# Optimization experiments

Measured on AMD Instinct MI355X. Metric: run time of the kernel, lower is better.

Reference implementation:

```python
import jax, jax.numpy as jnp
import numpy as np

B, S, D, H, T = 128, 256, 256, 1024, 128  # batch, src_len, input/output_dim, hidden, target_len


def setup_inputs() -> dict:
    key = jax.random.key(0)
    ks = jax.random.split(key, 16)
    sc = 0.05

    def p(k, shape):
        return (jax.random.normal(k, shape, jnp.float32) * sc)

    return {
        "x": jax.random.normal(ks[0], (B, S, D), jnp.float32),
        "x_target": jax.random.normal(ks[1], (B, T, D), jnp.float32),
        # encoder bidirectional LSTM (1 layer): gates order i,f,g,o (PyTorch)
        "enc_Wih_f": p(ks[2], (4 * H, D)),  "enc_Whh_f": p(ks[3], (4 * H, H)), "enc_b_f": p(ks[4], (4 * H,)),
        "enc_Wih_b": p(ks[5], (4 * H, D)),  "enc_Whh_b": p(ks[6], (4 * H, H)), "enc_b_b": p(ks[7], (4 * H,)),
        # decoder bidirectional LSTM (1 layer)
        "dec_Wih_f": p(ks[8], (4 * H, D)),  "dec_Whh_f": p(ks[9], (4 * H, H)), "dec_b_f": p(ks[10], (4 * H,)),
        "dec_Wih_b": p(ks[11], (4 * H, D)), "dec_Whh_b": p(ks[12], (4 * H, H)), "dec_b_b": p(ks[13], (4 * H,)),
        # decoder head: Linear(2H -> D)
        "mlp_W": p(ks[14], (D, 2 * H)), "mlp_b": p(ks[15], (D,)),
    }


def lstm_cell(x, h, c, Wih, Whh, b):
    # x: [B, Din], h/c: [B, H]; PyTorch gate order i, f, g, o
    g = x @ Wih.T + h @ Whh.T + b
    i, f, gg, o = jnp.split(g, 4, axis=-1)
    c = jax.nn.sigmoid(f) * c + jax.nn.sigmoid(i) * jnp.tanh(gg)
    h = jax.nn.sigmoid(o) * jnp.tanh(c)
    return h, c


def run_dir(xs, Wih, Whh, b, reverse):
    # xs: [S, B, Din]; returns final (h, c) for one direction (zero init, like torch LSTM without h0)
    h0 = jnp.zeros((xs.shape[1], Whh.shape[1]), xs.dtype)
    c0 = jnp.zeros_like(h0)

    def step(carry, xt):
        h, c = lstm_cell(xt, *carry, Wih, Whh, b)
        return (h, c), None

    (h, c), _ = jax.lax.scan(step, (h0, c0), xs, reverse=reverse)
    return h, c


def reference(x, x_target, enc_Wih_f, enc_Whh_f, enc_b_f, enc_Wih_b, enc_Whh_b, enc_b_b,
              dec_Wih_f, dec_Whh_f, dec_b_f, dec_Wih_b, dec_Whh_b, dec_b_b, mlp_W, mlp_b):
    xs = jnp.transpose(x, (1, 0, 2))  # [S, B, D], time-major
    hf, cf = run_dir(xs, enc_Wih_f, enc_Whh_f, enc_b_f, reverse=False)
    hb, cb = run_dir(xs, enc_Wih_b, enc_Whh_b, enc_b_b, reverse=True)

    dec_in = x[:, -1, :]  # [B, D]

    def step(carry, _):
        hf, cf, hb, cb, inp = carry
        # bidirectional LSTM on a length-1 sequence: both directions see the same step
        hf2, cf2 = lstm_cell(inp, hf, cf, dec_Wih_f, dec_Whh_f, dec_b_f)
        hb2, cb2 = lstm_cell(inp, hb, cb, dec_Wih_b, dec_Whh_b, dec_b_b)
        out = jnp.concatenate([hf2, hb2], axis=-1) @ mlp_W.T + mlp_b  # [B, D]
        # teacher_forcing_ratio = 0.0 -> always feed model output back
        return (hf2, cf2, hb2, cb2, out), out

    _, outs = jax.lax.scan(step, (hf, cf, hb, cb, dec_in), None, length=T)
    return jnp.transpose(outs, (1, 0, 2))  # [B, T, D]
```

## Files before the change

kernel.cpp:

```cpp
#include <hip/hip_runtime.h>
#include <stdint.h>


typedef __attribute__((ext_vector_type(8))) short bfx8;
typedef __attribute__((ext_vector_type(4))) float f32x4;
typedef __attribute__((ext_vector_type(4))) unsigned short u16x4;
typedef unsigned short ushort_t;
typedef unsigned long long u64;

#define NWG 256
#define MFMA(a,b,c) __builtin_amdgcn_mfma_f32_16x16x32_bf16((a),(b),(c),0,0,0)
#define WAITVM(N) { asm volatile("s_waitcnt vmcnt(" #N ")" ::: "memory"); __builtin_amdgcn_sched_barrier(0); }
#define WAITLG(N) { asm volatile("s_waitcnt lgkmcnt(" #N ")" ::: "memory"); __builtin_amdgcn_sched_barrier(0); }
#define SBAR()    { __builtin_amdgcn_s_barrier(); __builtin_amdgcn_sched_barrier(0); }

__device__ __forceinline__ unsigned short f2bf(float f){
  unsigned u = __float_as_uint(f);
  u += 0x7FFFu + ((u >> 16) & 1u);
  return (unsigned short)(u >> 16);
}
__device__ __forceinline__ float bf2f(unsigned short h){
  return __uint_as_float(((unsigned)h) << 16);
}
__device__ __forceinline__ float sigm(float x){ return 1.f/(1.f + __expf(-x)); }
__device__ __forceinline__ float tanh_(float x){ return 1.f - 2.f/(__expf(2.f*x) + 1.f); }

__device__ __forceinline__ void stage16(const void* g, void* l){
  __builtin_amdgcn_global_load_lds((const __attribute__((address_space(1))) void*)g,
                                   (__attribute__((address_space(3))) void*)l,
                                   16, 0, 0);
}
__device__ __forceinline__ void stage16c(const void* g, void* l){
  __builtin_amdgcn_global_load_lds((const __attribute__((address_space(1))) void*)g,
                                   (__attribute__((address_space(3))) void*)l,
                                   16, 0, 0x11);
}

__device__ __forceinline__ bfx8 ld16c(const ushort_t* p){
  const u64* q = (const u64*)p;
  u64 a = __hip_atomic_load(q,     __ATOMIC_RELAXED, __HIP_MEMORY_SCOPE_AGENT);
  u64 b = __hip_atomic_load(q + 1, __ATOMIC_RELAXED, __HIP_MEMORY_SCOPE_AGENT);
  union { u64 u[2]; bfx8 v; } x; x.u[0] = a; x.u[1] = b; return x.v;
}
__device__ __forceinline__ void sth2(ushort_t* p, unsigned short v){
  __hip_atomic_store(p, v, __ATOMIC_RELAXED, __HIP_MEMORY_SCOPE_AGENT);
}

__device__ __forceinline__ void cvt2(const f32x4& a, const f32x4& b, bfx8& hi, bfx8& lo){
#pragma unroll
  for (int j = 0; j < 4; ++j){
    unsigned short h0 = f2bf(a[j]);
    unsigned short h1 = f2bf(b[j]);
    hi[j]   = (short)h0; lo[j]   = (short)f2bf(a[j] - bf2f(h0));
    hi[4+j] = (short)h1; lo[4+j] = (short)f2bf(b[j] - bf2f(h1));
  }
}

__device__ __forceinline__ void bar(unsigned* flags, int nflags, int me, unsigned gen){
  __syncthreads();
  if (threadIdx.x == 0)
    __hip_atomic_store(&flags[me], gen, __ATOMIC_RELAXED, __HIP_MEMORY_SCOPE_AGENT);
  if (threadIdx.x < 64){
    const int l = threadIdx.x;
    for (;;){
      unsigned mn = 0xFFFFFFFFu;
      for (int o = l; o < nflags; o += 64){
        unsigned v = __hip_atomic_load(&flags[o], __ATOMIC_RELAXED, __HIP_MEMORY_SCOPE_AGENT);
        mn = mn < v ? mn : v;
      }
      if (__all((int)(mn >= gen))) break;
      __builtin_amdgcn_s_sleep(1);
    }
  }
  __syncthreads();
}

struct Frags { bfx8 awh0, awh1, awl0, awl1, bh0, bh1, bl0, bl1; };

template<int ENC>
__device__ __forceinline__ void cell_step(
    const float*    __restrict__ Wih,
    const ushort_t* __restrict__ WhH,
    const ushort_t* __restrict__ WhL,
    const float*    __restrict__ bias,
    const float*    __restrict__ xsl,
    const ushort_t* __restrict__ iph,
    const ushort_t* __restrict__ ipl,
    const ushort_t* __restrict__ hh,
    const ushort_t* __restrict__ hl,
    ushort_t* __restrict__ outh, ushort_t* __restrict__ outl,
    float (&creg)[2][2],
    int r0, int n0, int b0, ushort_t* LDS)
{
  const int tid  = threadIdx.x;
  const int lane = tid & 63;
  const int wv   = tid >> 6;
  const int wm   = wv >> 1, wn = wv & 1;
  const int lr   = tid >> 3;
  const int lc   = tid & 7;
  const int cb   = lane >> 4;
  const int fr   = lane & 15;
  const int sc8  = lc ^ (lr & 7);
  const int sx   = fr & 7;
  const int rwa0 = wm*32 + fr, rwa1 = rwa0 + 16;
  const int rwb0 = wn*32 + fr, rwb1 = rwb0 + 16;

  const int ra = r0 + lr, rb = ra + 32;
  const float* wih0 = Wih + (size_t)((ra & 3)*1024 + (ra >> 2))*256 + sc8*8;
  const float* wih1 = Wih + (size_t)((rb & 3)*1024 + (rb >> 2))*256 + sc8*8;
  const float *xs0 = nullptr, *xs1 = nullptr;
  const ushort_t *ih0 = nullptr, *ih1 = nullptr, *il0 = nullptr, *il1 = nullptr;
  if (ENC){
    xs0 = xsl + (size_t)(b0 + lr)*65536 + sc8*8;
    xs1 = xs0 + (size_t)32*65536;
  } else {
    ih0 = iph + (size_t)(b0 + lr)*256 + sc8*8;  ih1 = ih0 + 32*256;
    il0 = ipl + (size_t)(b0 + lr)*256 + sc8*8;  il1 = il0 + 32*256;
  }

  const ushort_t* sb; size_t sstr; int srow0;
  if      (wv == 0){ sb = WhH; sstr = 1024; srow0 = r0; }
  else if (wv == 1){ sb = WhL; sstr = 1024; srow0 = r0; }
  else if (wv == 2){ sb = hh;  sstr = 2048; srow0 = b0; }
  else             { sb = hl;  sstr = 2048; srow0 = b0; }
  const int srw = lane >> 3;
  const int sg  = (lane & 7) ^ srw;
  const ushort_t* pj[8];
#pragma unroll
  for (int j = 0; j < 8; ++j)
    pj[j] = sb + (size_t)(srow0 + j*8 + srw)*sstr + sg*8;
  ushort_t* ldsb[3];
#pragma unroll
  for (int bp = 0; bp < 3; ++bp)
    ldsb[bp] = LDS + 16384 + bp*16384 + wv*4096;

  auto ISSUE = [&](int c, int bp){
    const int ko = (c - 4)*64;
    if (wv < 2){
#pragma unroll
      for (int j = 0; j < 8; ++j)
        stage16(pj[j] + ko, ldsb[bp] + j*512);
    } else {
#pragma unroll
      for (int j = 0; j < 8; ++j)
        stage16c(pj[j] + ko, ldsb[bp] + j*512);
    }
  };

  f32x4 acc[2][2] = {};
  auto rdf = [&](const ushort_t* buf, int ks, Frags& f){
    const int ga = (((ks << 2) + cb) ^ sx) << 3;
    f.awh0 = *(const bfx8*)(buf +         rwa0*64 + ga);
    f.awh1 = *(const bfx8*)(buf +         rwa1*64 + ga);
    f.awl0 = *(const bfx8*)(buf + 4096  + rwa0*64 + ga);
    f.awl1 = *(const bfx8*)(buf + 4096  + rwa1*64 + ga);
    f.bh0  = *(const bfx8*)(buf + 8192  + rwb0*64 + ga);
    f.bh1  = *(const bfx8*)(buf + 8192  + rwb1*64 + ga);
    f.bl0  = *(const bfx8*)(buf + 12288 + rwb0*64 + ga);
    f.bl1  = *(const bfx8*)(buf + 12288 + rwb1*64 + ga);
  };
  auto mm12 = [&](const Frags& f){
    acc[0][0] = MFMA(f.awh0, f.bh0, acc[0][0]);
    acc[0][0] = MFMA(f.awh0, f.bl0, acc[0][0]);
    acc[0][0] = MFMA(f.awl0, f.bh0, acc[0][0]);
    acc[0][1] = MFMA(f.awh0, f.bh1, acc[0][1]);
    acc[0][1] = MFMA(f.awh0, f.bl1, acc[0][1]);
    acc[0][1] = MFMA(f.awl0, f.bh1, acc[0][1]);
    acc[1][0] = MFMA(f.awh1, f.bh0, acc[1][0]);
    acc[1][0] = MFMA(f.awh1, f.bl0, acc[1][0]);
    acc[1][0] = MFMA(f.awl1, f.bh0, acc[1][0]);
    acc[1][1] = MFMA(f.awh1, f.bh1, acc[1][1]);
    acc[1][1] = MFMA(f.awh1, f.bl1, acc[1][1]);
    acc[1][1] = MFMA(f.awl1, f.bh1, acc[1][1]);
  };

  f32x4 rw0a, rw0b, rw1a, rw1b, rxa0, rxb0, rxa1, rxb1;
  bfx8 cwh0, cwh1, cwl0, cwl1, cah0, cah1, cal0, cal1;
  auto LOADRAW = [&](int kc){
    rw0a = *(const f32x4*)(wih0 + kc);  rw0b = *(const f32x4*)(wih0 + kc + 4);
    rw1a = *(const f32x4*)(wih1 + kc);  rw1b = *(const f32x4*)(wih1 + kc + 4);
    if (ENC){
      rxa0 = *(const f32x4*)(xs0 + kc); rxb0 = *(const f32x4*)(xs0 + kc + 4);
      rxa1 = *(const f32x4*)(xs1 + kc); rxb1 = *(const f32x4*)(xs1 + kc + 4);
    } else {
      cah0 = ld16c(ih0 + kc);  cah1 = ld16c(ih1 + kc);
      cal0 = ld16c(il0 + kc);  cal1 = ld16c(il1 + kc);
    }
  };
  auto CVT = [&](){
    cvt2(rw0a, rw0b, cwh0, cwl0);
    cvt2(rw1a, rw1b, cwh1, cwl1);
    if (ENC){ cvt2(rxa0, rxb0, cah0, cal0); cvt2(rxa1, rxb1, cah1, cal1); }
  };

  LOADRAW(0);
  ISSUE(4, 0); ISSUE(5, 1); ISSUE(6, 2);
  CVT();

  for (int c = 0; c < 4; ++c){
    *(bfx8*)(LDS +         lr    *64 + lc*8) = cwh0;
    *(bfx8*)(LDS +        (lr+32)*64 + lc*8) = cwh1;
    *(bfx8*)(LDS + 4096 +  lr    *64 + lc*8) = cwl0;
    *(bfx8*)(LDS + 4096 + (lr+32)*64 + lc*8) = cwl1;
    *(bfx8*)(LDS + 8192 +  lr    *64 + lc*8) = cah0;
    *(bfx8*)(LDS + 8192 + (lr+32)*64 + lc*8) = cah1;
    *(bfx8*)(LDS + 12288 + lr    *64 + lc*8) = cal0;
    *(bfx8*)(LDS + 12288 +(lr+32)*64 + lc*8) = cal1;
    WAITLG(0); SBAR();
    if (c < 3) LOADRAW((c + 1)*64);
    Frags f0, f1;
    rdf(LDS, 0, f0);
    rdf(LDS, 1, f1);
    WAITLG(8);
    mm12(f0);
    WAITLG(0); SBAR();
    if (c < 3) CVT();
    mm12(f1);
  }

  int bi = 0;
  for (int i = 4; i <= 19; ++i){
    if (i < 18)      { WAITVM(16); }
    else if (i == 18){ WAITVM(8); }
    else             { WAITVM(0); }
    SBAR();
    const ushort_t* buf = LDS + 16384 + bi*16384;
    Frags f0, f1;
    rdf(buf, 0, f0);
    rdf(buf, 1, f1);
    WAITLG(8);
    mm12(f0);
    WAITLG(0); SBAR();
    if (i <= 16) ISSUE(i + 3, bi);
    mm12(f1);
    bi = (bi == 2) ? 0 : bi + 1;
  }

#pragma unroll
  for (int m = 0; m < 2; ++m){
    const int n = n0 + wm*8 + m*4 + cb;
    const float bi_ = bias[n];
    const float bf_ = bias[1024 + n];
    const float bg_ = bias[2048 + n];
    const float bo_ = bias[3072 + n];
#pragma unroll
    for (int nb = 0; nb < 2; ++nb){
      const int b = b0 + wn*32 + nb*16 + fr;
      float gi = acc[m][nb][0] + bi_;
      float gf = acc[m][nb][1] + bf_;
      float gg = acc[m][nb][2] + bg_;
      float go = acc[m][nb][3] + bo_;
      float c_new = sigm(gf)*creg[m][nb] + sigm(gi)*tanh_(gg);
      float h_new = sigm(go)*tanh_(c_new);
      creg[m][nb] = c_new;
      unsigned short hi = f2bf(h_new);
      sth2(&outh[(size_t)b*2048 + n], hi);
      sth2(&outl[(size_t)b*2048 + n], f2bf(h_new - bf2f(hi)));
    }
  }
}

__device__ __forceinline__ void mlp_gemm(
    const ushort_t* __restrict__ hch, const ushort_t* __restrict__ hcl,
    const ushort_t* __restrict__ mWh, const ushort_t* __restrict__ mWl,
    float* __restrict__ Part, int wg, ushort_t* LDS)
{
  const int tid = threadIdx.x, lane = tid & 63, wv = tid >> 6;
  const int cb = lane >> 4, fr = lane & 15, sx = fr & 7;
  const int wgl = wg & 127, kh = wg >> 7;
  const int d0 = (wgl >> 3)*16, b0 = (wgl & 7)*16;
  const int kb = kh*1024 + wv*256;
  const int srw = lane >> 3, sg = (lane & 7) ^ srw;

  const ushort_t* ps[4] = { mWh, mWl, hch, hcl };
  const int pr0[4] = { d0, d0, b0, b0 };
  const ushort_t* pj[4][2];
#pragma unroll
  for (int p = 0; p < 4; ++p)
#pragma unroll
    for (int j = 0; j < 2; ++j)
      pj[p][j] = ps[p] + (size_t)(pr0[p] + j*8 + srw)*2048 + kb + sg*8;
  ushort_t* lb[3];
#pragma unroll
  for (int bp = 0; bp < 3; ++bp)
    lb[bp] = LDS + 16384 + (wv*3 + bp)*4096;

  auto ISSUE = [&](int c, int bp){
    const int ko = c*64;
#pragma unroll
    for (int p = 0; p < 4; ++p)
#pragma unroll
      for (int j = 0; j < 2; ++j){
        if (p < 2) stage16 (pj[p][j] + ko, lb[bp] + p*1024 + j*512);
        else       stage16c(pj[p][j] + ko, lb[bp] + p*1024 + j*512);
      }
  };
  ISSUE(0, 0); ISSUE(1, 1); ISSUE(2, 2);

  f32x4 acc = {};
  int bp = 0;
  for (int c = 0; c < 4; ++c){
    if (c < 2)      { WAITVM(16); }
    else if (c == 2){ WAITVM(8); }
    else            { WAITVM(0); }
    const ushort_t* B = lb[bp];
    const int ga0 = ((cb) ^ sx) << 3;
    const int ga1 = ((4 + cb) ^ sx) << 3;
    bfx8 wh0 = *(const bfx8*)(B +        fr*64 + ga0);
    bfx8 wl0 = *(const bfx8*)(B + 1024 + fr*64 + ga0);
    bfx8 ah0 = *(const bfx8*)(B + 2048 + fr*64 + ga0);
    bfx8 al0 = *(const bfx8*)(B + 3072 + fr*64 + ga0);
    bfx8 wh1 = *(const bfx8*)(B +        fr*64 + ga1);
    bfx8 wl1 = *(const bfx8*)(B + 1024 + fr*64 + ga1);
    bfx8 ah1 = *(const bfx8*)(B + 2048 + fr*64 + ga1);
    bfx8 al1 = *(const bfx8*)(B + 3072 + fr*64 + ga1);
    WAITLG(0);
    if (c == 0) ISSUE(3, 0);
    acc = MFMA(wh0, ah0, acc); acc = MFMA(wh0, al0, acc); acc = MFMA(wl0, ah0, acc);
    acc = MFMA(wh1, ah1, acc); acc = MFMA(wh1, al1, acc); acc = MFMA(wl1, ah1, acc);
    bp = (bp == 2) ? 0 : bp + 1;
  }
  u64* P8 = (u64*)Part;
  const size_t idx = (((size_t)wgl*2 + kh)*4 + wv)*64 + lane;
  u64 a = ((u64)__float_as_uint(acc[1]) << 32) | __float_as_uint(acc[0]);
  u64 b = ((u64)__float_as_uint(acc[3]) << 32) | __float_as_uint(acc[2]);
  __hip_atomic_store(&P8[2*idx],     a, __ATOMIC_RELAXED, __HIP_MEMORY_SCOPE_AGENT);
  __hip_atomic_store(&P8[2*idx + 1], b, __ATOMIC_RELAXED, __HIP_MEMORY_SCOPE_AGENT);
}

__device__ __forceinline__ void mlp_combine(
    const float* __restrict__ Part, const float* __restrict__ mb,
    float* __restrict__ dout,
    ushort_t* __restrict__ inph, ushort_t* __restrict__ inpl, int wg, int t)
{
  if (threadIdx.x >= 64) return;
  const int lane = threadIdx.x;
  const int d0 = (wg >> 3)*16, b0 = (wg & 7)*16;
  const int cb = lane >> 4, fr = lane & 15;
  const u64* P8 = (const u64*)Part;
  f32x4 s = {};
#pragma unroll
  for (int kh = 0; kh < 2; ++kh)
#pragma unroll
    for (int wv = 0; wv < 4; ++wv){
      const size_t idx = (((size_t)wg*2 + kh)*4 + wv)*64 + lane;
      u64 a = __hip_atomic_load(&P8[2*idx],     __ATOMIC_RELAXED, __HIP_MEMORY_SCOPE_AGENT);
      u64 b = __hip_atomic_load(&P8[2*idx + 1], __ATOMIC_RELAXED, __HIP_MEMORY_SCOPE_AGENT);
      s[0] += __uint_as_float((unsigned)a);
      s[1] += __uint_as_float((unsigned)(a >> 32));
      s[2] += __uint_as_float((unsigned)b);
      s[3] += __uint_as_float((unsigned)(b >> 32));
    }
  const int dr = d0 + cb*4, b = b0 + fr;
  s += *(const f32x4*)&mb[dr];
  *(f32x4*)&dout[((size_t)b*128 + t)*256 + dr] = s;
  u16x4 hv, lv;
#pragma unroll
  for (int j = 0; j < 4; ++j){
    hv[j] = f2bf(s[j]);
    lv[j] = f2bf(s[j] - bf2f(hv[j]));
  }
  union { u16x4 v; u64 u; } ch, cl; ch.v = hv; cl.v = lv;
  __hip_atomic_store((u64*)&inph[(size_t)b*256 + dr], ch.u, __ATOMIC_RELAXED, __HIP_MEMORY_SCOPE_AGENT);
  __hip_atomic_store((u64*)&inpl[(size_t)b*256 + dr], cl.u, __ATOMIC_RELAXED, __HIP_MEMORY_SCOPE_AGENT);
}

__device__ __forceinline__ void wg_decode(int wg, int& dir, int& r0, int& n0,
                                          int& b0, int& me){
  const int half = (wg >> 3) & 1;
  const int rgd  = (wg & 7) | ((wg >> 4) << 3);
  dir = rgd >> 6;
  const int rg = rgd & 63;
  r0 = rg * 64; n0 = rg * 16; b0 = half * 64;
  me = (rg << 1) | half;
}

__global__ void __launch_bounds__(256) rnn_enc_kernel(
    const float* __restrict__ Wih_f, const float* __restrict__ b_f,
    const float* __restrict__ Wih_b, const float* __restrict__ b_b,
    const ushort_t* __restrict__ WhhH, const ushort_t* __restrict__ WhhL,
    const float* __restrict__ x,
    ushort_t* __restrict__ Hh, ushort_t* __restrict__ Hl,
    float* __restrict__ C, unsigned* flagsE)
{
  extern __shared__ ushort_t LDS[];
  int dir, r0, n0, b0, me;
  wg_decode(blockIdx.x, dir, r0, n0, b0, me);
  const float* Wih = dir ? Wih_b : Wih_f;
  const float* bia = dir ? b_b : b_f;
  const ushort_t* WhH = WhhH + (size_t)dir*4096*1024;
  const ushort_t* WhL = WhhL + (size_t)dir*4096*1024;
  unsigned* fl = flagsE + dir*128;
  float creg[2][2] = {{0.f, 0.f}, {0.f, 0.f}};
  unsigned gen = 0;
  for (int t = 0; t < 256; ++t){
    const int tt = dir ? (255 - t) : t;
    const int rp = t & 1;
    cell_step<1>(Wih, WhH, WhL, bia,
                 x + (size_t)tt*256, nullptr, nullptr,
                 Hh + (size_t)rp     *262144 + dir*1024,
                 Hl + (size_t)rp     *262144 + dir*1024,
                 Hh + (size_t)(rp^1) *262144 + dir*1024,
                 Hl + (size_t)(rp^1) *262144 + dir*1024,
                 creg, r0, n0, b0, LDS);
    ++gen;
    bar(fl, 128, me, gen);
  }
  {
    const int lane = threadIdx.x & 63, wv = threadIdx.x >> 6;
    const int wm = wv >> 1, wn = wv & 1, cb = lane >> 4, fr = lane & 15;
    float* Cst = C + (size_t)dir*1024*128;
#pragma unroll
    for (int m = 0; m < 2; ++m)
#pragma unroll
      for (int nb = 0; nb < 2; ++nb){
        const int n = n0 + wm*8 + m*4 + cb;
        const int b = b0 + wn*32 + nb*16 + fr;
        Cst[n*128 + b] = creg[m][nb];
      }
  }
}

__global__ void __launch_bounds__(256) rnn_dec_kernel(
    const float* __restrict__ Wih_f, const float* __restrict__ b_f,
    const float* __restrict__ Wih_b, const float* __restrict__ b_b,
    const ushort_t* __restrict__ WhhH, const ushort_t* __restrict__ WhhL,
    const ushort_t* __restrict__ mWh, const ushort_t* __restrict__ mWl,
    const float* __restrict__ mb,
    ushort_t* __restrict__ Hh, ushort_t* __restrict__ Hl,
    float* __restrict__ C,
    ushort_t* __restrict__ inph, ushort_t* __restrict__ inpl,
    float* __restrict__ Part,
    float* __restrict__ dout, unsigned* flagsD)
{
  extern __shared__ ushort_t LDS[];
  const int wg = blockIdx.x;
  int dir, r0, n0, b0, me;
  wg_decode(wg, dir, r0, n0, b0, me);
  const float* Wih = dir ? Wih_b : Wih_f;
  const float* bia = dir ? b_b : b_f;
  const ushort_t* WhH = WhhH + (size_t)dir*4096*1024;
  const ushort_t* WhL = WhhL + (size_t)dir*4096*1024;
  float creg[2][2];
  {
    const int lane = threadIdx.x & 63, wv = threadIdx.x >> 6;
    const int wm = wv >> 1, wn = wv & 1, cb = lane >> 4, fr = lane & 15;
    const float* Cst = C + (size_t)dir*1024*128;
#pragma unroll
    for (int m = 0; m < 2; ++m)
#pragma unroll
      for (int nb = 0; nb < 2; ++nb){
        const int n = n0 + wm*8 + m*4 + cb;
        const int b = b0 + wn*32 + nb*16 + fr;
        creg[m][nb] = Cst[n*128 + b];
      }
  }
  for (int t = 0; t < 128; ++t){
    const int rp = t & 1;
    cell_step<0>(Wih, WhH, WhL, bia,
                 nullptr, inph, inpl,
                 Hh + (size_t)rp     *262144 + dir*1024,
                 Hl + (size_t)rp     *262144 + dir*1024,
                 Hh + (size_t)(rp^1) *262144 + dir*1024,
                 Hl + (size_t)(rp^1) *262144 + dir*1024,
                 creg, r0, n0, b0, LDS);
    bar(flagsD, 256, wg, (unsigned)(3*t + 1));
    mlp_gemm(Hh + (size_t)(rp^1)*262144, Hl + (size_t)(rp^1)*262144,
             mWh, mWl, Part, wg, LDS);
    bar(flagsD, 256, wg, (unsigned)(3*t + 2));
    if (wg < 128) mlp_combine(Part, mb, dout, inph, inpl, wg, t);
    bar(flagsD, 256, wg, (unsigned)(3*t + 3));
  }
}

__global__ void k_wplanes(ushort_t* Hp, ushort_t* Lp,
                          const float* Whh_f, const float* Whh_b)
{
  const size_t N = 2ull*4096*1024;
  for (size_t i = (size_t)blockIdx.x*blockDim.x + threadIdx.x; i < N;
       i += (size_t)gridDim.x*blockDim.x){
    int dir = (int)(i >> 22);
    int r   = (int)((i >> 10) & 4095);
    int k   = (int)(i & 1023);
    int n = r >> 2, q = r & 3;
    const float* W = dir ? Whh_b : Whh_f;
    float v = W[(size_t)(q*1024 + n)*1024 + k];
    unsigned short h = f2bf(v);
    Hp[i] = h;
    Lp[i] = f2bf(v - bf2f(h));
  }
}

__global__ void k_init(ushort_t* Hh, ushort_t* Hl,
                       ushort_t* inph, ushort_t* inpl,
                       ushort_t* mWh, ushort_t* mWl,
                       const float* x, const float* mW, unsigned* cnt)
{
  const size_t N = 524288;
  for (size_t i = (size_t)blockIdx.x*blockDim.x + threadIdx.x; i < N;
       i += (size_t)gridDim.x*blockDim.x){
    Hh[i] = 0; Hl[i] = 0;
    float wv = mW[i];
    unsigned short wh = f2bf(wv);
    mWh[i] = wh;
    mWl[i] = f2bf(wv - bf2f(wh));
    if (i < 32768){
      int b = (int)(i >> 8), d = (int)(i & 255);
      float v = x[((size_t)b*256 + 255)*256 + d];
      unsigned short hi = f2bf(v);
      inph[i] = hi;
      inpl[i] = f2bf(v - bf2f(hi));
    }
    if (i < 1024) cnt[i] = 0;
  }
}

extern "C" void kernel_launch(void* const* d_in, const int* in_sizes, int n_in,
                              void* d_out, int out_size, void* d_ws, size_t ws_size,
                              hipStream_t stream)
{
  (void)in_sizes; (void)n_in; (void)out_size; (void)ws_size;
  const float* x      = (const float*)d_in[0];
  const float* eWih_f = (const float*)d_in[2];
  const float* eWhh_f = (const float*)d_in[3];
  const float* eb_f   = (const float*)d_in[4];
  const float* eWih_b = (const float*)d_in[5];
  const float* eWhh_b = (const float*)d_in[6];
  const float* eb_b   = (const float*)d_in[7];
  const float* dWih_f = (const float*)d_in[8];
  const float* dWhh_f = (const float*)d_in[9];
  const float* db_f   = (const float*)d_in[10];
  const float* dWih_b = (const float*)d_in[11];
  const float* dWhh_b = (const float*)d_in[12];
  const float* db_b   = (const float*)d_in[13];
  const float* mW     = (const float*)d_in[14];
  const float* mb     = (const float*)d_in[15];

  char* p = (char*)d_ws;
  size_t off = 0;
  unsigned* cnt   = (unsigned*)(p + off);  off += 4096;
  ushort_t* WhhEh = (ushort_t*)(p + off);  off += 16777216;
  ushort_t* WhhEl = (ushort_t*)(p + off);  off += 16777216;
  ushort_t* WhhDh = (ushort_t*)(p + off);  off += 16777216;
  ushort_t* WhhDl = (ushort_t*)(p + off);  off += 16777216;
  ushort_t* mWh   = (ushort_t*)(p + off);  off += 1048576;
  ushort_t* mWl   = (ushort_t*)(p + off);  off += 1048576;
  ushort_t* Hh    = (ushort_t*)(p + off);  off += 1048576;
  ushort_t* Hl    = (ushort_t*)(p + off);  off += 1048576;
  float*    C     = (float*)(p + off);     off += 1048576;
  ushort_t* inph  = (ushort_t*)(p + off);  off += 65536;
  ushort_t* inpl  = (ushort_t*)(p + off);  off += 65536;
  float*    Part  = (float*)(p + off);     off += 1048576;

  unsigned* flagsD = cnt;
  unsigned* flagsE = cnt + 256;

  hipFuncSetAttribute(reinterpret_cast<const void*>(rnn_enc_kernel),
                      hipFuncAttributeMaxDynamicSharedMemorySize, 131072);
  hipFuncSetAttribute(reinterpret_cast<const void*>(rnn_dec_kernel),
                      hipFuncAttributeMaxDynamicSharedMemorySize, 131072);

  k_init   <<<512, 256, 0, stream>>>(Hh, Hl, inph, inpl, mWh, mWl, x, mW, cnt);
  k_wplanes<<<2048, 256, 0, stream>>>(WhhEh, WhhEl, eWhh_f, eWhh_b);
  k_wplanes<<<2048, 256, 0, stream>>>(WhhDh, WhhDl, dWhh_f, dWhh_b);

  rnn_enc_kernel<<<NWG, 256, 131072, stream>>>(eWih_f, eb_f, eWih_b, eb_b,
                                               WhhEh, WhhEl, x, Hh, Hl, C, flagsE);
  rnn_dec_kernel<<<NWG, 256, 131072, stream>>>(dWih_f, db_f, dWih_b, db_b,
                                               WhhDh, WhhDl, mWh, mWl, mb,
                                               Hh, Hl, C, inph, inpl, Part,
                                               (float*)d_out, flagsD);
}
```

Before: 10.12 ms.

## Replicate hidden state into per-XCC scratch copies to avoid coherent cross-die loads

New measurement: 24.89 ms. 2.46x slower.

```diff
diff --git a/kernel.cpp b/kernel.cpp
--- a/kernel.cpp
+++ b/kernel.cpp
@@ -34,6 +34,11 @@
   __builtin_amdgcn_global_load_lds((const __attribute__((address_space(1))) void*)g,
                                    (__attribute__((address_space(3))) void*)l,
                                    16, 0, 0x11);
+}
+__device__ __forceinline__ void stage16s(const void* g, void* l){
+  __builtin_amdgcn_global_load_lds((const __attribute__((address_space(1))) void*)g,
+                                   (__attribute__((address_space(3))) void*)l,
+                                   16, 0, 0x1);
 }
 
 __device__ __forceinline__ bfx8 ld16c(const ushort_t* p){
@@ -75,9 +80,71 @@
   __syncthreads();
 }
 
+__device__ __forceinline__ void xreg(unsigned* regc, int grp, int& xcc, int& rank){
+  __shared__ unsigned s0, s1;
+  if (threadIdx.x == 0){
+    unsigned x;
+    asm volatile("s_getreg_b32 %0, hwreg(HW_REG_XCC_ID)" : "=s"(x));
+    x &= 7u;
+    s0 = x;
+    s1 = atomicAdd(&regc[(grp*8 + (int)x)*16], 1u);
+  }
+  __syncthreads();
+  xcc = (int)s0; rank = (int)s1;
+}
+__device__ __forceinline__ int xnmem(unsigned* regc, int grp, int xcc){
+  __shared__ unsigned s;
+  if (threadIdx.x == 0)
+    s = __hip_atomic_load(&regc[(grp*8 + xcc)*16], __ATOMIC_RELAXED, __HIP_MEMORY_SCOPE_AGENT);
+  __syncthreads();
+  return (int)s;
+}
+__device__ __forceinline__ void xbar(unsigned* arr, unsigned* flag, int nmem, unsigned gen){
+  __syncthreads();
+  if (threadIdx.x == 0){
+    unsigned a = atomicAdd(arr, 1u);
+    if (a == gen*(unsigned)nmem - 1u)
+      __hip_atomic_store(flag, gen, __ATOMIC_RELAXED, __HIP_MEMORY_SCOPE_AGENT);
+    while (__hip_atomic_load(flag, __ATOMIC_RELAXED, __HIP_MEMORY_SCOPE_AGENT) < gen)
+      __builtin_amdgcn_s_sleep(1);
+  }
+  __syncthreads();
+}
+
+__device__ __forceinline__ void xcopy_half(
+    const ushort_t* Hs, const ushort_t* Ls, ushort_t* Hd, ushort_t* Ld,
+    int dir, int rank, int nmem){
+  for (int u = rank*256 + (int)threadIdx.x; u < 16384; u += nmem*256){
+    const size_t o = (size_t)(u >> 7)*2048 + (size_t)dir*1024 + (size_t)(u & 127)*8;
+    const u64* s1 = (const u64*)(Hs + o);
+    const u64* s2 = (const u64*)(Ls + o);
+    u64 a = __hip_atomic_load(s1,     __ATOMIC_RELAXED, __HIP_MEMORY_SCOPE_AGENT);
+    u64 b = __hip_atomic_load(s1 + 1, __ATOMIC_RELAXED, __HIP_MEMORY_SCOPE_AGENT);
+    u64 c = __hip_atomic_load(s2,     __ATOMIC_RELAXED, __HIP_MEMORY_SCOPE_AGENT);
+    u64 d = __hip_atomic_load(s2 + 1, __ATOMIC_RELAXED, __HIP_MEMORY_SCOPE_AGENT);
+    ((u64*)(Hd + o))[0] = a; ((u64*)(Hd + o))[1] = b;
+    ((u64*)(Ld + o))[0] = c; ((u64*)(Ld + o))[1] = d;
+  }
+}
+__device__ __forceinline__ void xcopy_full(
+    const ushort_t* Hs, const ushort_t* Ls, ushort_t* Hd, ushort_t* Ld,
+    int rank, int nmem){
+  for (int u = rank*256 + (int)threadIdx.x; u < 32768; u += nmem*256){
+    const size_t o = (size_t)u*8;
+    const u64* s1 = (const u64*)(Hs + o);
+    const u64* s2 = (const u64*)(Ls + o);
+    u64 a = __hip_atomic_load(s1,     __ATOMIC_RELAXED, __HIP_MEMORY_SCOPE_AGENT);
+    u64 b = __hip_atomic_load(s1 + 1, __ATOMIC_RELAXED, __HIP_MEMORY_SCOPE_AGENT);
+    u64 c = __hip_atomic_load(s2,     __ATOMIC_RELAXED, __HIP_MEMORY_SCOPE_AGENT);
+    u64 d = __hip_atomic_load(s2 + 1, __ATOMIC_RELAXED, __HIP_MEMORY_SCOPE_AGENT);
+    ((u64*)(Hd + o))[0] = a; ((u64*)(Hd + o))[1] = b;
+    ((u64*)(Ld + o))[0] = c; ((u64*)(Ld + o))[1] = d;
+  }
+}
+
 struct Frags { bfx8 awh0, awh1, awl0, awl1, bh0, bh1, bl0, bl1; };
 
-template<int ENC>
+template<int ENC, int COH>
 __device__ __forceinline__ void cell_step(
     const float*    __restrict__ Wih,
     const ushort_t* __restrict__ WhH,
@@ -140,10 +207,14 @@
 #pragma unroll
       for (int j = 0; j < 8; ++j)
         stage16(pj[j] + ko, ldsb[bp] + j*512);
-    } else {
+    } else if (COH){
 #pragma unroll
       for (int j = 0; j < 8; ++j)
         stage16c(pj[j] + ko, ldsb[bp] + j*512);
+    } else {
+#pragma unroll
+      for (int j = 0; j < 8; ++j)
+        stage16s(pj[j] + ko, ldsb[bp] + j*512);
     }
   };
 
@@ -292,7 +363,7 @@
 #pragma unroll
       for (int j = 0; j < 2; ++j){
         if (p < 2) stage16 (pj[p][j] + ko, lb[bp] + p*1024 + j*512);
-        else       stage16c(pj[p][j] + ko, lb[bp] + p*1024 + j*512);
+        else       stage16s(pj[p][j] + ko, lb[bp] + p*1024 + j*512);
       }
   };
   ISSUE(0, 0); ISSUE(1, 1); ISSUE(2, 2);
@@ -381,7 +452,9 @@
     const ushort_t* __restrict__ WhhH, const ushort_t* __restrict__ WhhL,
     const float* __restrict__ x,
     ushort_t* __restrict__ Hh, ushort_t* __restrict__ Hl,
-    float* __restrict__ C, unsigned* flagsE)
+    ushort_t* __restrict__ scrH, ushort_t* __restrict__ scrL,
+    float* __restrict__ C, unsigned* flagsE,
+    unsigned* eReg, unsigned* eArr, unsigned* eFlg)
 {
   extern __shared__ ushort_t LDS[];
   int dir, r0, n0, b0, me;
@@ -391,20 +464,32 @@
   const ushort_t* WhH = WhhH + (size_t)dir*4096*1024;
   const ushort_t* WhL = WhhL + (size_t)dir*4096*1024;
   unsigned* fl = flagsE + dir*128;
+
+  int xcc, rank;
+  xreg(eReg, dir, xcc, rank);
+  bar(fl, 128, me, 1);
+  const int nmem = xnmem(eReg, dir, xcc);
+  const ushort_t* sH = scrH + (size_t)xcc*262144;
+  const ushort_t* sL = scrL + (size_t)xcc*262144;
+  unsigned* xa = eArr + (dir*8 + xcc)*16;
+  unsigned* xf = eFlg + (dir*8 + xcc)*16;
+
   float creg[2][2] = {{0.f, 0.f}, {0.f, 0.f}};
-  unsigned gen = 0;
   for (int t = 0; t < 256; ++t){
     const int tt = dir ? (255 - t) : t;
     const int rp = t & 1;
-    cell_step<1>(Wih, WhH, WhL, bia,
-                 x + (size_t)tt*256, nullptr, nullptr,
-                 Hh + (size_t)rp     *262144 + dir*1024,
-                 Hl + (size_t)rp     *262144 + dir*1024,
-                 Hh + (size_t)(rp^1) *262144 + dir*1024,
-                 Hl + (size_t)(rp^1) *262144 + dir*1024,
-                 creg, r0, n0, b0, LDS);
-    ++gen;
-    bar(fl, 128, me, gen);
+    cell_step<1,0>(Wih, WhH, WhL, bia,
+                   x + (size_t)tt*256, nullptr, nullptr,
+                   sH + dir*1024, sL + dir*1024,
+                   Hh + (size_t)(rp^1)*262144 + dir*1024,
+                   Hl + (size_t)(rp^1)*262144 + dir*1024,
+                   creg, r0, n0, b0, LDS);
+    bar(fl, 128, me, (unsigned)(t + 2));
+    if (t < 255){
+      xcopy_half(Hh + (size_t)(rp^1)*262144, Hl + (size_t)(rp^1)*262144,
+                 (ushort_t*)sH, (ushort_t*)sL, dir, rank, nmem);
+      xbar(xa, xf, nmem, (unsigned)(t + 1));
+    }
   }
   {
     const int lane = threadIdx.x & 63, wv = threadIdx.x >> 6;
@@ -428,10 +513,12 @@
     const ushort_t* __restrict__ mWh, const ushort_t* __restrict__ mWl,
     const float* __restrict__ mb,
     ushort_t* __restrict__ Hh, ushort_t* __restrict__ Hl,
+    ushort_t* __restrict__ scrH, ushort_t* __restrict__ scrL,
     float* __restrict__ C,
     ushort_t* __restrict__ inph, ushort_t* __restrict__ inpl,
     float* __restrict__ Part,
-    float* __restrict__ dout, unsigned* flagsD)
+    float* __restrict__ dout, unsigned* flagsD,
+    unsigned* dReg, unsigned* dArr, unsigned* dFlg)
 {
   extern __shared__ ushort_t LDS[];
   const int wg = blockIdx.x;
@@ -441,6 +528,16 @@
   const float* bia = dir ? b_b : b_f;
   const ushort_t* WhH = WhhH + (size_t)dir*4096*1024;
   const ushort_t* WhL = WhhL + (size_t)dir*4096*1024;
+
+  int xcc, rank;
+  xreg(dReg, 0, xcc, rank);
+  bar(flagsD, 256, wg, 1);
+  const int nmem = xnmem(dReg, 0, xcc);
+  const ushort_t* sH = scrH + (size_t)xcc*262144;
+  const ushort_t* sL = scrL + (size_t)xcc*262144;
+  unsigned* xa = dArr + xcc*16;
+  unsigned* xf = dFlg + xcc*16;
+
   float creg[2][2];
   {
     const int lane = threadIdx.x & 63, wv = threadIdx.x >> 6;
@@ -457,19 +554,27 @@
   }
   for (int t = 0; t < 128; ++t){
     const int rp = t & 1;
-    cell_step<0>(Wih, WhH, WhL, bia,
-                 nullptr, inph, inpl,
-                 Hh + (size_t)rp     *262144 + dir*1024,
-                 Hl + (size_t)rp     *262144 + dir*1024,
-                 Hh + (size_t)(rp^1) *262144 + dir*1024,
-                 Hl + (size_t)(rp^1) *262144 + dir*1024,
-                 creg, r0, n0, b0, LDS);
-    bar(flagsD, 256, wg, (unsigned)(3*t + 1));
-    mlp_gemm(Hh + (size_t)(rp^1)*262144, Hl + (size_t)(rp^1)*262144,
-             mWh, mWl, Part, wg, LDS);
+    if (t == 0)
+      cell_step<0,1>(Wih, WhH, WhL, bia, nullptr, inph, inpl,
+                     Hh + (size_t)rp*262144 + dir*1024,
+                     Hl + (size_t)rp*262144 + dir*1024,
+                     Hh + (size_t)(rp^1)*262144 + dir*1024,
+                     Hl + (size_t)(rp^1)*262144 + dir*1024,
+                     creg, r0, n0, b0, LDS);
+    else
+      cell_step<0,0>(Wih, WhH, WhL, bia, nullptr, inph, inpl,
+                     sH + dir*1024, sL + dir*1024,
+                     Hh + (size_t)(rp^1)*262144 + dir*1024,
+                     Hl + (size_t)(rp^1)*262144 + dir*1024,
+                     creg, r0, n0, b0, LDS);
     bar(flagsD, 256, wg, (unsigned)(3*t + 2));
+    xcopy_full(Hh + (size_t)(rp^1)*262144, Hl + (size_t)(rp^1)*262144,
+               (ushort_t*)sH, (ushort_t*)sL, rank, nmem);
+    xbar(xa, xf, nmem, (unsigned)(t + 1));
+    mlp_gemm(sH, sL, mWh, mWl, Part, wg, LDS);
+    bar(flagsD, 256, wg, (unsigned)(3*t + 3));
     if (wg < 128) mlp_combine(Part, mb, dout, inph, inpl, wg, t);
-    bar(flagsD, 256, wg, (unsigned)(3*t + 3));
+    bar(flagsD, 256, wg, (unsigned)(3*t + 4));
   }
 }
 
@@ -494,16 +599,20 @@
 __global__ void k_init(ushort_t* Hh, ushort_t* Hl,
                        ushort_t* inph, ushort_t* inpl,
                        ushort_t* mWh, ushort_t* mWl,
+                       ushort_t* scrH, ushort_t* scrL,
                        const float* x, const float* mW, unsigned* cnt)
 {
-  const size_t N = 524288;
+  const size_t N = 2097152;
   for (size_t i = (size_t)blockIdx.x*blockDim.x + threadIdx.x; i < N;
        i += (size_t)gridDim.x*blockDim.x){
-    Hh[i] = 0; Hl[i] = 0;
-    float wv = mW[i];
-    unsigned short wh = f2bf(wv);
-    mWh[i] = wh;
-    mWl[i] = f2bf(wv - bf2f(wh));
+    scrH[i] = 0; scrL[i] = 0;
+    if (i < 524288){
+      Hh[i] = 0; Hl[i] = 0;
+      float wv = mW[i];
+      unsigned short wh = f2bf(wv);
+      mWh[i] = wh;
+      mWl[i] = f2bf(wv - bf2f(wh));
+    }
     if (i < 32768){
       int b = (int)(i >> 8), d = (int)(i & 255);
       float v = x[((size_t)b*256 + 255)*256 + d];
@@ -511,7 +620,7 @@
       inph[i] = hi;
       inpl[i] = f2bf(v - bf2f(hi));
     }
-    if (i < 1024) cnt[i] = 0;
+    if (i < 2048) cnt[i] = 0;
   }
 }
 
@@ -538,7 +647,7 @@
 
   char* p = (char*)d_ws;
   size_t off = 0;
-  unsigned* cnt   = (unsigned*)(p + off);  off += 4096;
+  unsigned* cnt   = (unsigned*)(p + off);  off += 8192;
   ushort_t* WhhEh = (ushort_t*)(p + off);  off += 16777216;
   ushort_t* WhhEl = (ushort_t*)(p + off);  off += 16777216;
   ushort_t* WhhDh = (ushort_t*)(p + off);  off += 16777216;
@@ -551,23 +660,36 @@
   ushort_t* inph  = (ushort_t*)(p + off);  off += 65536;
   ushort_t* inpl  = (ushort_t*)(p + off);  off += 65536;
   float*    Part  = (float*)(p + off);     off += 1048576;
+  ushort_t* scrH  = (ushort_t*)(p + off);  off += 4194304;
+  ushort_t* scrL  = (ushort_t*)(p + off);  off += 4194304;
 
   unsigned* flagsD = cnt;
   unsigned* flagsE = cnt + 256;
+  unsigned* eReg   = cnt + 512;
+  unsigned* eArr   = cnt + 768;
+  unsigned* eFlg   = cnt + 1024;
+  unsigned* dReg   = cnt + 1280;
+  unsigned* dArr   = cnt + 1408;
+  unsigned* dFlg   = cnt + 1536;
 
   hipFuncSetAttribute(reinterpret_cast<const void*>(rnn_enc_kernel),
                       hipFuncAttributeMaxDynamicSharedMemorySize, 131072);
   hipFuncSetAttribute(reinterpret_cast<const void*>(rnn_dec_kernel),
                       hipFuncAttributeMaxDynamicSharedMemorySize, 131072);
 
-  k_init   <<<512, 256, 0, stream>>>(Hh, Hl, inph, inpl, mWh, mWl, x, mW, cnt);
+  k_init   <<<512, 256, 0, stream>>>(Hh, Hl, inph, inpl, mWh, mWl,
+                                     scrH, scrL, x, mW, cnt);
   k_wplanes<<<2048, 256, 0, stream>>>(WhhEh, WhhEl, eWhh_f, eWhh_b);
   k_wplanes<<<2048, 256, 0, stream>>>(WhhDh, WhhDl, dWhh_f, dWhh_b);
 
   rnn_enc_kernel<<<NWG, 256, 131072, stream>>>(eWih_f, eb_f, eWih_b, eb_b,
-                                               WhhEh, WhhEl, x, Hh, Hl, C, flagsE);
+                                               WhhEh, WhhEl, x, Hh, Hl,
+                                               scrH, scrL, C, flagsE,
+                                               eReg, eArr, eFlg);
   rnn_dec_kernel<<<NWG, 256, 131072, stream>>>(dWih_f, db_f, dWih_b, db_b,
                                                WhhDh, WhhDl, mWh, mWl, mb,
-                                               Hh, Hl, C, inph, inpl, Part,
-                                               (float*)d_out, flagsD);
-}
+                                               Hh, Hl, scrH, scrL, C,
+                                               inph, inpl, Part,
+                                               (float*)d_out, flagsD,
+                                               dReg, dArr, dFlg);
+}
```

## Prefetch recurrent weights across barriers and fuse MLP head into fewer WGs

Applied to the files above, without the earlier changes.

New measurement: 10.22 ms. Within noise of the previous version (+1.0%).

```diff
diff --git a/kernel.cpp b/kernel.cpp
--- a/kernel.cpp
+++ b/kernel.cpp
@@ -73,6 +73,41 @@
     }
   }
   __syncthreads();
+}
+
+struct WPre {
+  const ushort_t* pj[8];
+  ushort_t* ldsb[3];
+  bool active;
+};
+__device__ __forceinline__ void wpre_issue(const WPre& w){
+  if (!w.active) return;
+#pragma unroll
+  for (int bp = 0; bp < 3; ++bp)
+#pragma unroll
+    for (int j = 0; j < 8; ++j)
+      stage16(w.pj[j] + bp*64, w.ldsb[bp] + j*512);
+}
+__device__ __forceinline__ void bar_pf(unsigned* flags, int nflags, int me,
+                                       unsigned gen, const WPre& w, bool pf){
+  WAITLG(0); WAITVM(0);
+  SBAR();
+  if (pf) wpre_issue(w);
+  if (threadIdx.x == 192)
+    __hip_atomic_store(&flags[me], gen, __ATOMIC_RELAXED, __HIP_MEMORY_SCOPE_AGENT);
+  if ((threadIdx.x >> 6) == 3){
+    const int l = threadIdx.x & 63;
+    for (;;){
+      unsigned mn = 0xFFFFFFFFu;
+      for (int o = l; o < nflags; o += 64){
+        unsigned v = __hip_atomic_load(&flags[o], __ATOMIC_RELAXED, __HIP_MEMORY_SCOPE_AGENT);
+        mn = mn < v ? mn : v;
+      }
+      if (__all((int)(mn >= gen))) break;
+      __builtin_amdgcn_s_sleep(1);
+    }
+  }
+  SBAR();
 }
 
 struct Frags { bfx8 awh0, awh1, awl0, awl1, bh0, bh1, bl0, bl1; };
@@ -194,7 +229,7 @@
   };
 
   LOADRAW(0);
-  ISSUE(4, 0); ISSUE(5, 1); ISSUE(6, 2);
+  if (wv >= 2){ ISSUE(4, 0); ISSUE(5, 1); ISSUE(6, 2); }
   CVT();
 
   for (int c = 0; c < 4; ++c){
@@ -260,109 +295,91 @@
   }
 }
 
-__device__ __forceinline__ void mlp_gemm(
+__device__ __forceinline__ void mlp32(
     const ushort_t* __restrict__ hch, const ushort_t* __restrict__ hcl,
     const ushort_t* __restrict__ mWh, const ushort_t* __restrict__ mWl,
-    float* __restrict__ Part, int wg, ushort_t* LDS)
+    const float* __restrict__ mb, float* __restrict__ dout,
+    ushort_t* __restrict__ inph, ushort_t* __restrict__ inpl,
+    int wg, int t, ushort_t* LDS)
 {
   const int tid = threadIdx.x, lane = tid & 63, wv = tid >> 6;
-  const int cb = lane >> 4, fr = lane & 15, sx = fr & 7;
-  const int wgl = wg & 127, kh = wg >> 7;
-  const int d0 = (wgl >> 3)*16, b0 = (wgl & 7)*16;
-  const int kb = kh*1024 + wv*256;
-  const int srw = lane >> 3, sg = (lane & 7) ^ srw;
-
-  const ushort_t* ps[4] = { mWh, mWl, hch, hcl };
-  const int pr0[4] = { d0, d0, b0, b0 };
-  const ushort_t* pj[4][2];
-#pragma unroll
-  for (int p = 0; p < 4; ++p)
-#pragma unroll
-    for (int j = 0; j < 2; ++j)
-      pj[p][j] = ps[p] + (size_t)(pr0[p] + j*8 + srw)*2048 + kb + sg*8;
-  ushort_t* lb[3];
-#pragma unroll
-  for (int bp = 0; bp < 3; ++bp)
-    lb[bp] = LDS + 16384 + (wv*3 + bp)*4096;
-
-  auto ISSUE = [&](int c, int bp){
-    const int ko = c*64;
-#pragma unroll
-    for (int p = 0; p < 4; ++p)
-#pragma unroll
-      for (int j = 0; j < 2; ++j){
-        if (p < 2) stage16 (pj[p][j] + ko, lb[bp] + p*1024 + j*512);
-        else       stage16c(pj[p][j] + ko, lb[bp] + p*1024 + j*512);
+  const int d0 = (wg >> 2)*32, b0 = (wg & 3)*32;
+  const int kb = wv*512;
+  const int srw2 = lane >> 2;
+  const int pg   = lane & 3;
+
+  const ushort_t* base[4] = { mWh, mWl, hch, hcl };
+  const int rb0[4] = { d0, d0, b0, b0 };
+  const ushort_t* sp[8];
+#pragma unroll
+  for (int j = 0; j < 8; ++j){
+    const int p = j >> 1, sub = j & 1;
+    const int rl = sub*16 + srw2;
+    const int sr = (rl ^ (rl >> 2)) & 3;
+    sp[j] = base[p] + (size_t)(rb0[p] + rl)*2048 + kb + ((pg ^ sr)*8);
+  }
+  ushort_t* lb[2] = { LDS + 16384 + wv*8192, LDS + 16384 + wv*8192 + 4096 };
+
+  auto MISSUE = [&](int c){
+    ushort_t* B = lb[c & 1];
+    const int ko = c*32;
+#pragma unroll
+    for (int j = 0; j < 8; ++j){
+      const int p = j >> 1, sub = j & 1;
+      if (p < 2) stage16 (sp[j] + ko, B + p*1024 + sub*512 + lane*8);
+      else       stage16c(sp[j] + ko, B + p*1024 + sub*512 + lane*8);
+    }
+  };
+  MISSUE(0); MISSUE(1);
+
+  f32x4 acc[2][2] = {};
+  const int lg = lane >> 4;
+  for (int c = 0; c < 16; ++c){
+    if (c < 15) { WAITVM(8); } else { WAITVM(0); }
+    const ushort_t* B = lb[c & 1];
+    bfx8 wf[2][2], af[2][2];
+#pragma unroll
+    for (int m = 0; m < 2; ++m){
+      const int rl = m*16 + (lane & 15);
+      const int sr = (rl ^ (rl >> 2)) & 3;
+      const int off = rl*32 + ((lg ^ sr)*8);
+      wf[0][m] = *(const bfx8*)(B + off);
+      wf[1][m] = *(const bfx8*)(B + 1024 + off);
+      af[0][m] = *(const bfx8*)(B + 2048 + off);
+      af[1][m] = *(const bfx8*)(B + 3072 + off);
+    }
+    WAITLG(0);
+    if (c < 14) MISSUE(c + 2);
+#pragma unroll
+    for (int m = 0; m < 2; ++m)
+#pragma unroll
+      for (int n = 0; n < 2; ++n){
+        acc[m][n] = MFMA(wf[0][m], af[0][n], acc[m][n]);
+        acc[m][n] = MFMA(wf[0][m], af[1][n], acc[m][n]);
+        acc[m][n] = MFMA(wf[1][m], af[0][n], acc[m][n]);
       }
-  };
-  ISSUE(0, 0); ISSUE(1, 1); ISSUE(2, 2);
-
-  f32x4 acc = {};
-  int bp = 0;
-  for (int c = 0; c < 4; ++c){
-    if (c < 2)      { WAITVM(16); }
-    else if (c == 2){ WAITVM(8); }
-    else            { WAITVM(0); }
-    const ushort_t* B = lb[bp];
-    const int ga0 = ((cb) ^ sx) << 3;
-    const int ga1 = ((4 + cb) ^ sx) << 3;
-    bfx8 wh0 = *(const bfx8*)(B +        fr*64 + ga0);
-    bfx8 wl0 = *(const bfx8*)(B + 1024 + fr*64 + ga0);
-    bfx8 ah0 = *(const bfx8*)(B + 2048 + fr*64 + ga0);
-    bfx8 al0 = *(const bfx8*)(B + 3072 + fr*64 + ga0);
-    bfx8 wh1 = *(const bfx8*)(B +        fr*64 + ga1);
-    bfx8 wl1 = *(const bfx8*)(B + 1024 + fr*64 + ga1);
-    bfx8 ah1 = *(const bfx8*)(B + 2048 + fr*64 + ga1);
-    bfx8 al1 = *(const bfx8*)(B + 3072 + fr*64 + ga1);
-    WAITLG(0);
-    if (c == 0) ISSUE(3, 0);
-    acc = MFMA(wh0, ah0, acc); acc = MFMA(wh0, al0, acc); acc = MFMA(wl0, ah0, acc);
-    acc = MFMA(wh1, ah1, acc); acc = MFMA(wh1, al1, acc); acc = MFMA(wl1, ah1, acc);
-    bp = (bp == 2) ? 0 : bp + 1;
-  }
-  u64* P8 = (u64*)Part;
-  const size_t idx = (((size_t)wgl*2 + kh)*4 + wv)*64 + lane;
-  u64 a = ((u64)__float_as_uint(acc[1]) << 32) | __float_as_uint(acc[0]);
-  u64 b = ((u64)__float_as_uint(acc[3]) << 32) | __float_as_uint(acc[2]);
-  __hip_atomic_store(&P8[2*idx],     a, __ATOMIC_RELAXED, __HIP_MEMORY_SCOPE_AGENT);
-  __hip_atomic_store(&P8[2*idx + 1], b, __ATOMIC_RELAXED, __HIP_MEMORY_SCOPE_AGENT);
-}
-
-__device__ __forceinline__ void mlp_combine(
-    const float* __restrict__ Part, const float* __restrict__ mb,
-    float* __restrict__ dout,
-    ushort_t* __restrict__ inph, ushort_t* __restrict__ inpl, int wg, int t)
-{
-  if (threadIdx.x >= 64) return;
-  const int lane = threadIdx.x;
-  const int d0 = (wg >> 3)*16, b0 = (wg & 7)*16;
-  const int cb = lane >> 4, fr = lane & 15;
-  const u64* P8 = (const u64*)Part;
-  f32x4 s = {};
-#pragma unroll
-  for (int kh = 0; kh < 2; ++kh)
-#pragma unroll
-    for (int wv = 0; wv < 4; ++wv){
-      const size_t idx = (((size_t)wg*2 + kh)*4 + wv)*64 + lane;
-      u64 a = __hip_atomic_load(&P8[2*idx],     __ATOMIC_RELAXED, __HIP_MEMORY_SCOPE_AGENT);
-      u64 b = __hip_atomic_load(&P8[2*idx + 1], __ATOMIC_RELAXED, __HIP_MEMORY_SCOPE_AGENT);
-      s[0] += __uint_as_float((unsigned)a);
-      s[1] += __uint_as_float((unsigned)(a >> 32));
-      s[2] += __uint_as_float((unsigned)b);
-      s[3] += __uint_as_float((unsigned)(b >> 32));
-    }
-  const int dr = d0 + cb*4, b = b0 + fr;
-  s += *(const f32x4*)&mb[dr];
-  *(f32x4*)&dout[((size_t)b*128 + t)*256 + dr] = s;
-  u16x4 hv, lv;
-#pragma unroll
-  for (int j = 0; j < 4; ++j){
-    hv[j] = f2bf(s[j]);
-    lv[j] = f2bf(s[j] - bf2f(hv[j]));
-  }
-  union { u16x4 v; u64 u; } ch, cl; ch.v = hv; cl.v = lv;
-  __hip_atomic_store((u64*)&inph[(size_t)b*256 + dr], ch.u, __ATOMIC_RELAXED, __HIP_MEMORY_SCOPE_AGENT);
-  __hip_atomic_store((u64*)&inpl[(size_t)b*256 + dr], cl.u, __ATOMIC_RELAXED, __HIP_MEMORY_SCOPE_AGENT);
+  }
+
+  float* PL = (float*)LDS;
+#pragma unroll
+  for (int m = 0; m < 2; ++m)
+#pragma unroll
+    for (int n = 0; n < 2; ++n)
+#pragma unroll
+      for (int r = 0; r < 4; ++r)
+        PL[wv*1024 + (m*2 + n)*256 + r*64 + lane] = acc[m][n][r];
+  __syncthreads();
+  for (int o = tid; o < 1024; o += 256){
+    float s = PL[o] + PL[1024 + o] + PL[2048 + o] + PL[3072 + o];
+    const int m = o >> 9, n = (o >> 8) & 1, r = (o >> 6) & 3, l = o & 63;
+    const int d = d0 + m*16 + (l >> 4)*4 + r;
+    const int b = b0 + n*16 + (l & 15);
+    s += mb[d];
+    dout[((size_t)b*128 + t)*256 + d] = s;
+    const unsigned short hv = f2bf(s);
+    sth2(&inph[(size_t)b*256 + d], hv);
+    sth2(&inpl[(size_t)b*256 + d], f2bf(s - bf2f(hv)));
+  }
 }
 
 __device__ __forceinline__ void wg_decode(int wg, int& dir, int& r0, int& n0,
@@ -373,6 +390,23 @@
   const int rg = rgd & 63;
   r0 = rg * 64; n0 = rg * 16; b0 = half * 64;
   me = (rg << 1) | half;
+}
+
+__device__ __forceinline__ WPre make_wpre(const ushort_t* WhH, const ushort_t* WhL,
+                                          int r0, ushort_t* LDS){
+  const int tid = threadIdx.x, lane = tid & 63, wv = tid >> 6;
+  const int srw = lane >> 3;
+  const int sg  = (lane & 7) ^ srw;
+  WPre w;
+  w.active = (wv < 2);
+  const ushort_t* sb = (wv == 1) ? WhL : WhH;
+#pragma unroll
+  for (int j = 0; j < 8; ++j)
+    w.pj[j] = sb + (size_t)(r0 + j*8 + srw)*1024 + sg*8;
+#pragma unroll
+  for (int bp = 0; bp < 3; ++bp)
+    w.ldsb[bp] = LDS + 16384 + bp*16384 + wv*4096;
+  return w;
 }
 
 __global__ void __launch_bounds__(256) rnn_enc_kernel(
@@ -391,8 +425,10 @@
   const ushort_t* WhH = WhhH + (size_t)dir*4096*1024;
   const ushort_t* WhL = WhhL + (size_t)dir*4096*1024;
   unsigned* fl = flagsE + dir*128;
+  const WPre wp = make_wpre(WhH, WhL, r0, LDS);
+
   float creg[2][2] = {{0.f, 0.f}, {0.f, 0.f}};
-  unsigned gen = 0;
+  wpre_issue(wp);
   for (int t = 0; t < 256; ++t){
     const int tt = dir ? (255 - t) : t;
     const int rp = t & 1;
@@ -403,8 +439,7 @@
                  Hh + (size_t)(rp^1) *262144 + dir*1024,
                  Hl + (size_t)(rp^1) *262144 + dir*1024,
                  creg, r0, n0, b0, LDS);
-    ++gen;
-    bar(fl, 128, me, gen);
+    bar_pf(fl, 128, me, (unsigned)(t + 1), wp, t < 255);
   }
   {
     const int lane = threadIdx.x & 63, wv = threadIdx.x >> 6;
@@ -430,7 +465,6 @@
     ushort_t* __restrict__ Hh, ushort_t* __restrict__ Hl,
     float* __restrict__ C,
     ushort_t* __restrict__ inph, ushort_t* __restrict__ inpl,
-    float* __restrict__ Part,
     float* __restrict__ dout, unsigned* flagsD)
 {
   extern __shared__ ushort_t LDS[];
@@ -441,6 +475,8 @@
   const float* bia = dir ? b_b : b_f;
   const ushort_t* WhH = WhhH + (size_t)dir*4096*1024;
   const ushort_t* WhL = WhhL + (size_t)dir*4096*1024;
+  const WPre wp = make_wpre(WhH, WhL, r0, LDS);
+
   float creg[2][2];
   {
     const int lane = threadIdx.x & 63, wv = threadIdx.x >> 6;
@@ -455,6 +491,7 @@
         creg[m][nb] = Cst[n*128 + b];
       }
   }
+  wpre_issue(wp);
   for (int t = 0; t < 128; ++t){
     const int rp = t & 1;
     cell_step<0>(Wih, WhH, WhL, bia,
@@ -464,12 +501,11 @@
                  Hh + (size_t)(rp^1) *262144 + dir*1024,
                  Hl + (size_t)(rp^1) *262144 + dir*1024,
                  creg, r0, n0, b0, LDS);
-    bar(flagsD, 256, wg, (unsigned)(3*t + 1));
-    mlp_gemm(Hh + (size_t)(rp^1)*262144, Hl + (size_t)(rp^1)*262144,
-             mWh, mWl, Part, wg, LDS);
-    bar(flagsD, 256, wg, (unsigned)(3*t + 2));
-    if (wg < 128) mlp_combine(Part, mb, dout, inph, inpl, wg, t);
-    bar(flagsD, 256, wg, (unsigned)(3*t + 3));
+    bar(flagsD, 256, wg, (unsigned)(2*t + 1));
+    if (wg < 32)
+      mlp32(Hh + (size_t)(rp^1)*262144, Hl + (size_t)(rp^1)*262144,
+            mWh, mWl, mb, dout, inph, inpl, wg, t, LDS);
+    bar_pf(flagsD, 256, wg, (unsigned)(2*t + 2), wp, t < 127);
   }
 }
 
@@ -511,7 +547,7 @@
       inph[i] = hi;
       inpl[i] = f2bf(v - bf2f(hi));
     }
-    if (i < 1024) cnt[i] = 0;
+    if (i < 2048) cnt[i] = 0;
   }
 }
 
@@ -538,7 +574,7 @@
 
   char* p = (char*)d_ws;
   size_t off = 0;
-  unsigned* cnt   = (unsigned*)(p + off);  off += 4096;
+  unsigned* cnt   = (unsigned*)(p + off);  off += 8192;
   ushort_t* WhhEh = (ushort_t*)(p + off);  off += 16777216;
   ushort_t* WhhEl = (ushort_t*)(p + off);  off += 16777216;
   ushort_t* WhhDh = (ushort_t*)(p + off);  off += 16777216;
@@ -550,7 +586,6 @@
   float*    C     = (float*)(p + off);     off += 1048576;
   ushort_t* inph  = (ushort_t*)(p + off);  off += 65536;
   ushort_t* inpl  = (ushort_t*)(p + off);  off += 65536;
-  float*    Part  = (float*)(p + off);     off += 1048576;
 
   unsigned* flagsD = cnt;
   unsigned* flagsE = cnt + 256;
@@ -568,6 +603,6 @@
                                                WhhEh, WhhEl, x, Hh, Hl, C, flagsE);
   rnn_dec_kernel<<<NWG, 256, 131072, stream>>>(dWih_f, db_f, dWih_b, db_b,
                                                WhhDh, WhhDl, mWh, mWl, mb,
-                                               Hh, Hl, C, inph, inpl, Part,
+                                               Hh, Hl, C, inph, inpl,
                                                (float*)d_out, flagsD);
 }
```
